# Kernel tuning notes

Hardware: AMD Instinct MI355X
Metric: run time of the kernel (lower is better)

## Reference

```python
import jax, jax.numpy as jnp
import numpy as np

# MoE_Bottleneck constants from source
E = 4   # number of experts
K = 2   # top-k routing


def setup_inputs() -> dict:
    key = jax.random.key(0)
    ks = jax.random.split(key, 10)
    B, C1, H, W = 8, 256, 64, 64
    C2 = 256
    Ch = C2 // 2  # c_ = int(c2*0.5) = 128
    x = jax.random.normal(ks[0], (B, C1, H, W), dtype=jnp.float32)
    # Conv = conv2d(no bias)+BN+SiLU; BN folded into weight scale + bias (eval mode).
    W1 = jax.random.normal(ks[1], (Ch, C1), dtype=jnp.float32) / np.sqrt(C1)
    b1 = jax.random.normal(ks[2], (Ch,), dtype=jnp.float32) * 0.1
    Wr = jax.random.normal(ks[3], (E, Ch), dtype=jnp.float32) / np.sqrt(Ch)
    br = jax.random.normal(ks[4], (E,), dtype=jnp.float32) * 0.1
    # Expert Conv(c_, c_, 3, 1): full 3x3 kernels [E, Cout, Cin, 3, 3]
    We = jax.random.normal(ks[5], (E, Ch, Ch, 3, 3), dtype=jnp.float32) / np.sqrt(Ch * 9)
    be = jax.random.normal(ks[6], (E, Ch), dtype=jnp.float32) * 0.1
    W3 = jax.random.normal(ks[7], (C2, Ch), dtype=jnp.float32) / np.sqrt(Ch)
    b3 = jax.random.normal(ks[8], (C2,), dtype=jnp.float32) * 0.1
    return {"x": x, "W1": W1, "b1": b1, "Wr": Wr, "br": br,
            "We": We, "be": be, "W3": W3, "b3": b3}


def reference(x, W1, b1, Wr, br, We, be, W3, b3):
    silu = jax.nn.silu
    # conv1: 1x1 conv + (folded BN) + SiLU
    x_in = silu(jnp.einsum('bchw,oc->bohw', x, W1) + b1[None, :, None, None])
    B, C, H, Wd = x_in.shape
    N = B * H * Wd
    xr = x_in.transpose(0, 2, 3, 1).reshape(N, C)            # [N, C] tokens
    # router: 1x1 conv -> per-pixel logits over E experts
    logits = xr @ Wr.T + br                                   # [N, E]
    probs = jax.nn.softmax(logits, axis=-1)
    topw, topi = jax.lax.top_k(probs, K)                      # [N, K]
    topw = topw / jnp.sum(topw, axis=-1, keepdims=True)       # renormalize top-k
    # dense [N, E] routing-weight matrix (indices within a row are unique)
    wmat = jnp.zeros_like(probs).at[jnp.arange(N)[:, None], topi].set(topw)
    # Experts: 3x3 conv applied to 1x1 spatial patches with pad=1 -> only the
    # center tap We[..., 1, 1] contributes (padding is zeros). Folded-BN bias + SiLU.
    Wc = We[:, :, :, 1, 1]                                    # [E, Cout, Cin]
    eout = silu(jnp.einsum('nc,eoc->neo', xr, Wc) + be[None]) # [N, E, C]
    moe = jnp.einsum('neo,ne->no', eout, wmat)                # weighted combine
    out = moe.reshape(B, H, Wd, C).transpose(0, 3, 1, 2)
    # conv3: 1x1 conv + SiLU
    y = silu(jnp.einsum('bchw,oc->bohw', out, W3) + b3[None, :, None, None])
    # shortcut=True and c1 == c2
    return y + x
```

## Files before the change

### kernel.cpp

```cpp
#include <hip/hip_runtime.h>
#include <hip/hip_bf16.h>


typedef unsigned short u16;
typedef unsigned int   u32;
typedef __attribute__((ext_vector_type(8))) short short8;
typedef __attribute__((ext_vector_type(4))) float f32x4;

#define MFMA16 __builtin_amdgcn_mfma_f32_16x16x32_bf16

__device__ __forceinline__ float silu_f(float v) { return v / (1.0f + __expf(-v)); }
__device__ __forceinline__ u16 f2bf(float f) {
    u32 u = __float_as_uint(f);
    return (u16)((u + 0x7fff + ((u >> 16) & 1)) >> 16);
}
__device__ __forceinline__ float bf2f(u16 h) { return __uint_as_float(((u32)h) << 16); }
__device__ __forceinline__ u32 pkbf(float a, float b) {
    __hip_bfloat162 h2 = __float22bfloat162_rn(make_float2(a, b));
    u32 r; __builtin_memcpy(&r, &h2, 4); return r;
}
__device__ __forceinline__ int key3(int r) { return (r ^ (r >> 2)) & 7; }

__global__ void prep_weights(const float* __restrict__ W1,
                             const float* __restrict__ We,
                             const float* __restrict__ W3,
                             u16* __restrict__ ws)
{
    int idx = blockIdx.x * 256 + threadIdx.x;
    if (idx < 36864) {
        int kc = idx / 9216, r = idx % 9216;
        int n = r / 72, j = r % 72;
        float v = (j < 64) ? W1[n * 256 + kc * 64 + j] : 0.0f;
        u16 h = f2bf(v);
        float lo = v - bf2f(h);
        ws[idx] = h;
        ws[36864 + idx] = f2bf(lo);
    } else if (idx < 102400) {
        int i = idx - 36864;
        int e = i >> 14, r = i & 16383;
        int o = r >> 7, rem = r & 127;
        int ps = rem >> 3, t = rem & 7;
        int gi = (ps & 8) | ((ps ^ key3(o)) & 7);
        int c = gi * 8 + t;
        ws[73728 + i] = f2bf(We[(size_t)(((e * 128 + o) * 128 + c) * 9) + 4]);
    } else if (idx < 135168) {
        int i = idx - 102400;
        int h = i >> 14, r = i & 16383;
        int o = r >> 7, rem = r & 127;
        int ps = rem >> 3, t = rem & 7;
        int gi = (ps & 8) | ((ps ^ key3(o)) & 7);
        int c = gi * 8 + t;
        ws[139264 + i] = f2bf(W3[(size_t)(h * 128 + o) * 128 + c]);
    }
}

__device__ __forceinline__ void stage_chunk(const u16* __restrict__ g, u16* l, int tid) {
#pragma unroll
    for (int i = 0; i < 4; ++i)
        __builtin_amdgcn_global_load_lds(g + (size_t)(i * 512 + tid) * 8,
                                         l + (size_t)(i * 512 + (tid & 448)) * 8, 16, 0, 0);
}

__global__ __launch_bounds__(512, 4)
void fused_moe_mfma(const float* __restrict__ x,
                    const float* __restrict__ b1g,
                    const float* __restrict__ Wrg,
                    const float* __restrict__ brg,
                    const float* __restrict__ beg,
                    const float* __restrict__ b3g,
                    const u16* __restrict__ wbf,
                    float* __restrict__ out)
{
    __shared__ __align__(16) unsigned char smem[81920];
    u16*   const sWhi = (u16*)(smem);
    u16*   const sWlo = (u16*)(smem + 18432);
    u16*   const sAhi = (u16*)(smem + 36864);
    u16*   const sAlo = (u16*)(smem + 46080);
    u16*   const A2   = (u16*)(smem);
    u16*   const bufA = (u16*)(smem + 16384);
    u16*   const bufB = (u16*)(smem + 49152);
    float* const sLg  = (float*)(smem + 49152);
    float* const sY   = (float*)(smem + 16384);

    const int tid = threadIdx.x;
    const int l  = tid & 63;
    const int w  = tid >> 6;
    const int wm = w & 3, wn = w >> 2;
    const int lr = l & 15;
    const int g  = l >> 4;
    const int mrow = 16 * wm + 4 * g;
    const int arow = 16 * wm + lr;
    const int ak3 = key3(arow);
    int oc[4], ok3[4];
#pragma unroll
    for (int f = 0; f < 4; ++f) { oc[f] = 64 * wn + 16 * f + lr; ok3[f] = key3(oc[f]); }

    const int n0  = blockIdx.x << 6;
    const float* xb = x   + ((size_t)(n0 >> 12) * 256) * 4096 + (n0 & 4095);
    float*       ob = out + ((size_t)(n0 >> 12) * 256) * 4096 + (n0 & 4095);

    f32x4 acc1[4];
#pragma unroll
    for (int f = 0; f < 4; ++f) acc1[f] = (f32x4){0.f, 0.f, 0.f, 0.f};

    const int c2 = tid >> 4;
    const int m4 = (tid & 15) << 2;

#pragma unroll 1
    for (int kc = 0; kc < 4; ++kc) {
        __syncthreads();
        const float* xa = xb + (size_t)(kc * 64 + 2 * c2) * 4096 + m4;
        float4 fa = *(const float4*)xa;
        float4 fb = *(const float4*)(xa + 4096);
#pragma unroll
        for (int i = 0; i < 3; ++i) {
            int idx = i * 512 + tid;
            if (idx < 1152) {
                int ub = i * 512 + (tid & 448);
                __builtin_amdgcn_global_load_lds(wbf + (size_t)kc * 9216 + (size_t)idx * 8,
                                                 sWhi + (size_t)ub * 8, 16, 0, 0);
                __builtin_amdgcn_global_load_lds(wbf + (size_t)(36864 + kc * 9216) + (size_t)idx * 8,
                                                 sWlo + (size_t)ub * 8, 16, 0, 0);
            }
        }
        {
            u32* H = (u32*)sAhi; u32* L = (u32*)sAlo;
            float fav[4] = {fa.x, fa.y, fa.z, fa.w};
            float fbv[4] = {fb.x, fb.y, fb.z, fb.w};
#pragma unroll
            for (int r = 0; r < 4; ++r) {
                int row = m4 + r;
                u32 hi = pkbf(fav[r], fbv[r]);
                float la = fav[r] - __uint_as_float(hi << 16);
                float lb = fbv[r] - __uint_as_float(hi & 0xffff0000u);
                int jj = c2 ^ (key3(row) << 2);
                H[row * 36 + jj] = hi; L[row * 36 + jj] = pkbf(la, lb);
            }
        }
        __syncthreads();
#pragma unroll
        for (int ks = 0; ks < 2; ++ks) {
            int jb = (ks * 16 + g * 4) ^ (ak3 << 2);
            short8 ah = *(const short8*)&sAhi[arow * 72 + jb * 2];
            short8 al = *(const short8*)&sAlo[arow * 72 + jb * 2];
#pragma unroll
            for (int f = 0; f < 4; ++f) {
                int bo = oc[f] * 72 + ks * 32 + g * 8;
                short8 bh = *(const short8*)&sWhi[bo];
                short8 bl = *(const short8*)&sWlo[bo];
                acc1[f] = MFMA16(ah, bh, acc1[f], 0, 0, 0);
                acc1[f] = MFMA16(al, bh, acc1[f], 0, 0, 0);
                acc1[f] = MFMA16(ah, bl, acc1[f], 0, 0, 0);
                acc1[f] = MFMA16(al, bl, acc1[f], 0, 0, 0);
            }
        }
    }
    __syncthreads();
    stage_chunk(wbf + 73728, bufA, tid);

    float xin[4][4];
#pragma unroll
    for (int f = 0; f < 4; ++f) {
        float bias = b1g[oc[f]];
#pragma unroll
        for (int i = 0; i < 4; ++i) xin[f][i] = silu_f(acc1[f][i] + bias);
    }
#pragma unroll
    for (int f = 0; f < 4; ++f) {
        int c = oc[f], cg = c >> 3;
#pragma unroll
        for (int i = 0; i < 4; ++i) {
            int m = mrow + i;
            int ps = (cg & 8) | ((cg ^ key3(m)) & 7);
            A2[m * 128 + ps * 8 + (c & 7)] = f2bf(xin[f][i]);
        }
    }
    float lg[4][4];
#pragma unroll
    for (int e = 0; e < 4; ++e)
#pragma unroll
        for (int i = 0; i < 4; ++i) lg[e][i] = 0.f;
#pragma unroll
    for (int f = 0; f < 4; ++f) {
        int c = oc[f];
        float w0 = Wrg[c], w1 = Wrg[128 + c], w2 = Wrg[256 + c], w3 = Wrg[384 + c];
#pragma unroll
        for (int i = 0; i < 4; ++i) {
            float xv = xin[f][i];
            lg[0][i] += xv * w0; lg[1][i] += xv * w1;
            lg[2][i] += xv * w2; lg[3][i] += xv * w3;
        }
    }
#pragma unroll
    for (int d = 1; d < 16; d <<= 1)
#pragma unroll
        for (int e = 0; e < 4; ++e)
#pragma unroll
            for (int i = 0; i < 4; ++i)
                lg[e][i] += __shfl_xor(lg[e][i], d, 64);
    if (lr == 0) {
#pragma unroll
        for (int i = 0; i < 4; ++i)
#pragma unroll
            for (int e = 0; e < 4; ++e)
                sLg[(wn * 64 + mrow + i) * 4 + e] = lg[e][i];
    }
    __syncthreads();

    float br0 = brg[0], br1 = brg[1], br2 = brg[2], br3 = brg[3];
    float rw[4][4];
#pragma unroll
    for (int i = 0; i < 4; ++i) {
        int m = mrow + i;
        float le0 = sLg[m * 4 + 0] + sLg[(64 + m) * 4 + 0] + br0;
        float le1 = sLg[m * 4 + 1] + sLg[(64 + m) * 4 + 1] + br1;
        float le2 = sLg[m * 4 + 2] + sLg[(64 + m) * 4 + 2] + br2;
        float le3 = sLg[m * 4 + 3] + sLg[(64 + m) * 4 + 3] + br3;
        int c0 = (le1 > le0) + (le2 > le0) + (le3 > le0);
        int c1 = (le0 >= le1) + (le2 > le1) + (le3 > le1);
        int c2r = (le0 >= le2) + (le1 >= le2) + (le3 > le2);
        int c3 = (le0 >= le3) + (le1 >= le3) + (le2 >= le3);
        float m0 = fmaxf(fmaxf(le0, le1), fmaxf(le2, le3));
        float p0 = (c0 < 2) ? __expf(le0 - m0) : 0.f;
        float p1 = (c1 < 2) ? __expf(le1 - m0) : 0.f;
        float p2 = (c2r < 2) ? __expf(le2 - m0) : 0.f;
        float p3 = (c3 < 2) ? __expf(le3 - m0) : 0.f;
        float inv = 1.0f / (p0 + p1 + p2 + p3);
        rw[0][i] = p0 * inv; rw[1][i] = p1 * inv;
        rw[2][i] = p2 * inv; rw[3][i] = p3 * inv;
    }
    __syncthreads();
    stage_chunk(wbf + 73728 + 16384, bufB, tid);

    f32x4 macc[4];
#pragma unroll
    for (int f = 0; f < 4; ++f) macc[f] = (f32x4){0.f, 0.f, 0.f, 0.f};

#pragma unroll 1
    for (int e = 0; e < 4; ++e) {
        const u16* Wb = (e & 1) ? bufB : bufA;
        f32x4 acce[4];
#pragma unroll
        for (int f = 0; f < 4; ++f) acce[f] = (f32x4){0.f, 0.f, 0.f, 0.f};
#pragma unroll
        for (int ks = 0; ks < 4; ++ks) {
            int gi = ks * 4 + g;
            int psA = (gi & 8) | ((gi ^ ak3) & 7);
            short8 a = *(const short8*)&A2[arow * 128 + psA * 8];
#pragma unroll
            for (int f = 0; f < 4; ++f) {
                int psB = (gi & 8) | ((gi ^ ok3[f]) & 7);
                short8 bb = *(const short8*)&Wb[oc[f] * 128 + psB * 8];
                acce[f] = MFMA16(a, bb, acce[f], 0, 0, 0);
            }
        }
#pragma unroll
        for (int f = 0; f < 4; ++f) {
            float bias = beg[e * 128 + oc[f]];
#pragma unroll
            for (int i = 0; i < 4; ++i)
                macc[f][i] += rw[e][i] * silu_f(acce[f][i] + bias);
        }
        __syncthreads();
        if (e < 2)       stage_chunk(wbf + 73728 + (e + 2) * 16384, (e & 1) ? bufB : bufA, tid);
        else if (e == 2) stage_chunk(wbf + 139264, bufA, tid);
    }

#pragma unroll
    for (int f = 0; f < 4; ++f) {
        int c = oc[f], cg = c >> 3;
#pragma unroll
        for (int i = 0; i < 4; ++i) {
            int m = mrow + i;
            int ps = (cg & 8) | ((cg ^ key3(m)) & 7);
            A2[m * 128 + ps * 8 + (c & 7)] = f2bf(macc[f][i]);
        }
    }
    __syncthreads();
    stage_chunk(wbf + 139264 + 16384, bufB, tid);

#pragma unroll 1
    for (int h = 0; h < 2; ++h) {
        const u16* Wb = h ? bufB : bufA;
        f32x4 acc3[4];
#pragma unroll
        for (int f = 0; f < 4; ++f) acc3[f] = (f32x4){0.f, 0.f, 0.f, 0.f};
#pragma unroll
        for (int ks = 0; ks < 4; ++ks) {
            int gi = ks * 4 + g;
            int psA = (gi & 8) | ((gi ^ ak3) & 7);
            short8 a = *(const short8*)&A2[arow * 128 + psA * 8];
#pragma unroll
            for (int f = 0; f < 4; ++f) {
                int psB = (gi & 8) | ((gi ^ ok3[f]) & 7);
                short8 bb = *(const short8*)&Wb[oc[f] * 128 + psB * 8];
                acc3[f] = MFMA16(a, bb, acc3[f], 0, 0, 0);
            }
        }
        __syncthreads();
        int mg = mrow >> 2;
#pragma unroll
        for (int f = 0; f < 4; ++f) {
            int o = oc[f];
            float bias = b3g[h * 128 + o];
            float4 v;
            v.x = silu_f(acc3[f][0] + bias);
            v.y = silu_f(acc3[f][1] + bias);
            v.z = silu_f(acc3[f][2] + bias);
            v.w = silu_f(acc3[f][3] + bias);
            *(float4*)&sY[o * 64 + ((mg ^ ok3[f]) << 2)] = v;
        }
        __syncthreads();
#pragma unroll
        for (int q = 0; q < 4; ++q) {
            int idx = q * 512 + tid;
            int o = idx >> 4, mq = idx & 15;
            int og = h * 128 + o;
            float4 vy = *(const float4*)&sY[o * 64 + ((mq ^ key3(o)) << 2)];
            size_t goff = (size_t)og * 4096 + (mq << 2);
            float4 r = *(const float4*)&xb[goff];
            vy.x += r.x; vy.y += r.y; vy.z += r.z; vy.w += r.w;
            *(float4*)&ob[goff] = vy;
        }
        if (h == 0) __syncthreads();
    }
}

extern "C" void kernel_launch(void* const* d_in, const int* in_sizes, int n_in,
                              void* d_out, int out_size, void* d_ws, size_t ws_size,
                              hipStream_t stream)
{
    const float* x  = (const float*)d_in[0];
    const float* W1 = (const float*)d_in[1];
    const float* b1 = (const float*)d_in[2];
    const float* Wr = (const float*)d_in[3];
    const float* br = (const float*)d_in[4];
    const float* We = (const float*)d_in[5];
    const float* be = (const float*)d_in[6];
    const float* W3 = (const float*)d_in[7];
    const float* b3 = (const float*)d_in[8];
    float* outp = (float*)d_out;
    u16* wbf = (u16*)d_ws;

    hipLaunchKernelGGL(prep_weights, dim3(528), dim3(256), 0, stream,
                       W1, We, W3, wbf);
    hipLaunchKernelGGL(fused_moe_mfma, dim3(512), dim3(512), 0, stream,
                       x, b1, Wr, br, be, b3, wbf, outp);
}
```

Baseline: 51.11 us.

## Double-buffer conv1 K-loop with smaller chunks and prefetched x/W1 staging

```diff
diff --git a/kernel.cpp b/kernel.cpp
--- a/kernel.cpp
+++ b/kernel.cpp
@@ -28,13 +28,12 @@
 {
     int idx = blockIdx.x * 256 + threadIdx.x;
     if (idx < 36864) {
-        int kc = idx / 9216, r = idx % 9216;
-        int n = r / 72, j = r % 72;
-        float v = (j < 64) ? W1[n * 256 + kc * 64 + j] : 0.0f;
+        int kc = idx / 4608, q = idx % 4608;
+        int o = q / 36, j = q % 36;
+        float v = (j < 32) ? W1[o * 256 + kc * 32 + j] : 0.0f;
         u16 h = f2bf(v);
-        float lo = v - bf2f(h);
-        ws[idx] = h;
-        ws[36864 + idx] = f2bf(lo);
+        ws[kc * 9216 + q] = h;
+        ws[kc * 9216 + 4608 + q] = f2bf(v - bf2f(h));
     } else if (idx < 102400) {
         int i = idx - 36864;
         int e = i >> 14, r = i & 16383;
@@ -60,6 +59,15 @@
         __builtin_amdgcn_global_load_lds(g + (size_t)(i * 512 + tid) * 8,
                                          l + (size_t)(i * 512 + (tid & 448)) * 8, 16, 0, 0);
 }
+__device__ __forceinline__ void stageW1(const u16* __restrict__ g, u16* l, int tid) {
+#pragma unroll
+    for (int i = 0; i < 3; ++i) {
+        int u = i * 512 + tid;
+        if (u < 1152)
+            __builtin_amdgcn_global_load_lds(g + (size_t)u * 8,
+                                             l + (size_t)(i * 512 + (tid & 448)) * 8, 16, 0, 0);
+    }
+}
 
 __global__ __launch_bounds__(512, 4)
 void fused_moe_mfma(const float* __restrict__ x,
@@ -72,10 +80,10 @@
                     float* __restrict__ out)
 {
     __shared__ __align__(16) unsigned char smem[81920];
-    u16*   const sWhi = (u16*)(smem);
-    u16*   const sWlo = (u16*)(smem + 18432);
-    u16*   const sAhi = (u16*)(smem + 36864);
-    u16*   const sAlo = (u16*)(smem + 46080);
+    u16*   const Wb0 = (u16*)(smem);
+    u16*   const Wb1 = (u16*)(smem + 18432);
+    u16*   const Ab0 = (u16*)(smem + 36864);
+    u16*   const Ab1 = (u16*)(smem + 46080);
     u16*   const A2   = (u16*)(smem);
     u16*   const bufA = (u16*)(smem + 16384);
     u16*   const bufB = (u16*)(smem + 49152);
@@ -103,59 +111,63 @@
 #pragma unroll
     for (int f = 0; f < 4; ++f) acc1[f] = (f32x4){0.f, 0.f, 0.f, 0.f};
 
-    const int c2 = tid >> 4;
-    const int m4 = (tid & 15) << 2;
+    const int c2 = tid >> 5;
+    const int mp = (tid & 31) << 1;
+
+    {
+        float2 xe = *(const float2*)&xb[(size_t)(2 * c2) * 4096 + mp];
+        float2 xo = *(const float2*)&xb[(size_t)(2 * c2 + 1) * 4096 + mp];
+        stageW1(wbf, Wb0, tid);
+        u32* H = (u32*)Ab0; u32* L = (u32*)(Ab0 + 2304);
+        float fe[2] = {xe.x, xe.y}, fo[2] = {xo.x, xo.y};
+#pragma unroll
+        for (int r = 0; r < 2; ++r) {
+            u32 hi = pkbf(fe[r], fo[r]);
+            float la = fe[r] - __uint_as_float(hi << 16);
+            float lb = fo[r] - __uint_as_float(hi & 0xffff0000u);
+            H[(mp + r) * 18 + c2] = hi; L[(mp + r) * 18 + c2] = pkbf(la, lb);
+        }
+    }
+    __syncthreads();
 
 #pragma unroll 1
-    for (int kc = 0; kc < 4; ++kc) {
-        __syncthreads();
-        const float* xa = xb + (size_t)(kc * 64 + 2 * c2) * 4096 + m4;
-        float4 fa = *(const float4*)xa;
-        float4 fb = *(const float4*)(xa + 4096);
-#pragma unroll
-        for (int i = 0; i < 3; ++i) {
-            int idx = i * 512 + tid;
-            if (idx < 1152) {
-                int ub = i * 512 + (tid & 448);
-                __builtin_amdgcn_global_load_lds(wbf + (size_t)kc * 9216 + (size_t)idx * 8,
-                                                 sWhi + (size_t)ub * 8, 16, 0, 0);
-                __builtin_amdgcn_global_load_lds(wbf + (size_t)(36864 + kc * 9216) + (size_t)idx * 8,
-                                                 sWlo + (size_t)ub * 8, 16, 0, 0);
-            }
+    for (int kc = 0; kc < 8; ++kc) {
+        float2 ne, no;
+        if (kc < 7) {
+            ne = *(const float2*)&xb[(size_t)((kc + 1) * 32 + 2 * c2) * 4096 + mp];
+            no = *(const float2*)&xb[(size_t)((kc + 1) * 32 + 2 * c2 + 1) * 4096 + mp];
+            stageW1(wbf + (kc + 1) * 9216, (kc & 1) ? Wb0 : Wb1, tid);
         }
         {
-            u32* H = (u32*)sAhi; u32* L = (u32*)sAlo;
-            float fav[4] = {fa.x, fa.y, fa.z, fa.w};
-            float fbv[4] = {fb.x, fb.y, fb.z, fb.w};
-#pragma unroll
-            for (int r = 0; r < 4; ++r) {
-                int row = m4 + r;
-                u32 hi = pkbf(fav[r], fbv[r]);
-                float la = fav[r] - __uint_as_float(hi << 16);
-                float lb = fbv[r] - __uint_as_float(hi & 0xffff0000u);
-                int jj = c2 ^ (key3(row) << 2);
-                H[row * 36 + jj] = hi; L[row * 36 + jj] = pkbf(la, lb);
-            }
-        }
-        __syncthreads();
-#pragma unroll
-        for (int ks = 0; ks < 2; ++ks) {
-            int jb = (ks * 16 + g * 4) ^ (ak3 << 2);
-            short8 ah = *(const short8*)&sAhi[arow * 72 + jb * 2];
-            short8 al = *(const short8*)&sAlo[arow * 72 + jb * 2];
+            const u16* Ab = (kc & 1) ? Ab1 : Ab0;
+            const u16* Wv = (kc & 1) ? Wb1 : Wb0;
+            short8 ah = *(const short8*)&Ab[arow * 36 + g * 8];
+            short8 al = *(const short8*)&Ab[2304 + arow * 36 + g * 8];
 #pragma unroll
             for (int f = 0; f < 4; ++f) {
-                int bo = oc[f] * 72 + ks * 32 + g * 8;
-                short8 bh = *(const short8*)&sWhi[bo];
-                short8 bl = *(const short8*)&sWlo[bo];
+                const u16* bp = &Wv[oc[f] * 36 + g * 8];
+                short8 bh = *(const short8*)bp;
+                short8 bl = *(const short8*)(bp + 4608);
                 acc1[f] = MFMA16(ah, bh, acc1[f], 0, 0, 0);
                 acc1[f] = MFMA16(al, bh, acc1[f], 0, 0, 0);
                 acc1[f] = MFMA16(ah, bl, acc1[f], 0, 0, 0);
                 acc1[f] = MFMA16(al, bl, acc1[f], 0, 0, 0);
             }
         }
-    }
-    __syncthreads();
+        if (kc < 7) {
+            u16* Ax = (kc & 1) ? Ab0 : Ab1;
+            u32* H = (u32*)Ax; u32* L = (u32*)(Ax + 2304);
+            float fe[2] = {ne.x, ne.y}, fo[2] = {no.x, no.y};
+#pragma unroll
+            for (int r = 0; r < 2; ++r) {
+                u32 hi = pkbf(fe[r], fo[r]);
+                float la = fe[r] - __uint_as_float(hi << 16);
+                float lb = fo[r] - __uint_as_float(hi & 0xffff0000u);
+                H[(mp + r) * 18 + c2] = hi; L[(mp + r) * 18 + c2] = pkbf(la, lb);
+            }
+        }
+        __syncthreads();
+    }
     stage_chunk(wbf + 73728, bufA, tid);
 
     float xin[4][4];
```

Result: slower. 79.17 us (+54.9%).
